# Kernel optimization log

Measured on AMD Instinct MI355X. Metric: run time of the kernel, lower is better.

Reference implementation:

```python
import jax, jax.numpy as jnp
import numpy as np

B, SST, SL = 16, 256, 48
VOCAB, D, CH = 16384, 64, 112
TPI = 0.0


def setup_inputs() -> dict:
    key = jax.random.key(0)
    ks = jax.random.split(key, 26)
    def n(k, shp, s=0.05):
        return jax.random.normal(k, shp, dtype=jnp.float32) * s
    return {
        "x": jax.random.randint(ks[0], (B, SST), 0, VOCAB),
        "ees": n(ks[1], (B, D, SL), 1.0),
        "emb": n(ks[2], (VOCAB, D)),
        "cl0_w": n(ks[3], (CH, D, 1)),  "cl0_b": n(ks[4], (CH,)),
        "cl1_w": n(ks[5], (CH, CH, 3)), "cl1_b": n(ks[6], (CH,)),
        "claa_w": n(ks[7], (CH, CH, 3)), "claa_b": n(ks[8], (CH,)),
        "clfa_w": n(ks[9], (CH, CH, 3)), "clfa_b": n(ks[10], (CH,)),
        "ccac_w": n(ks[11], (CH, CH, 3)), "ccac_b": n(ks[12], (CH,)),
        "cib_w": n(ks[13], (D, CH, 1)),  "cib_b": n(ks[14], (D,)),
        "cpr1_w": n(ks[15], (D, 2 * D, 1)), "cpr1_b": n(ks[16], (D,)),
        "cpr2_w": n(ks[17], (D, D, 1)),  "cpr2_b": n(ks[18], (D,)),
        "cma_w": n(ks[19], (CH, D, 1)),  "cma_b": n(ks[20], (CH,)),
        "ccf_w": n(ks[21], (D, CH, 1)),  "ccf_b": n(ks[22], (D,)),
        "fff_b": n(ks[23], (VOCAB,)),
    }


def _conv1x1(x, w, b):
    # x: [B,C,S], w: [O,C,1] -> [B,O,S]
    return jnp.einsum('oc,bcs->bos', w[:, :, 0], x) + b[None, :, None]


def _conv3(x, w, b):
    # valid 1D conv, channels-first. x: [B,C,S+2] -> [B,O,S]
    y = jax.lax.conv_general_dilated(x, w, (1,), 'VALID',
                                     dimension_numbers=('NCH', 'OIH', 'NCH'))
    return y + b[None, :, None]


def _forward(x, ees, emb, cl0_w, cl0_b, cl1_w, cl1_b, claa_w, claa_b,
             clfa_w, clfa_b, ccac_w, ccac_b, cib_w, cib_b,
             cpr1_w, cpr1_b, cpr2_w, cpr2_b, cma_w, cma_b,
             ccf_w, ccf_b, fff_b):
    b = x.shape[0]
    pre_d = jnp.transpose(emb[x], (0, 2, 1))            # [B,64,SST]
    t = _conv1x1(pre_d, cl0_w, cl0_b)                   # [B,112,SST]
    tp = jnp.full((b, CH, 2), TPI, dtype=t.dtype)       # tpi pad columns

    # split cpr layer1 weight into the t-half and ees-half (concat along ch)
    wt, we = cpr1_w[:, :D, 0], cpr1_w[:, D:, 0]

    def stage(t_in, conv_w, conv_b):
        tt = jnp.concatenate([tp, t_in], axis=2)        # [B,112,SST+2]
        xconv = jax.nn.relu(_conv3(tt, conv_w, conv_b))  # [B,112,SST]
        c = _conv1x1(xconv, cib_w, cib_b)               # [B,64,SST]
        # all-pairs broadcast (sl x sst) + 1x1-conv MLP, equivalent to
        # repeat/concat/cpr in the original, without duplicating data
        h = (jnp.einsum('oc,bcs->bos', wt, c)[:, :, None, :]
             + jnp.einsum('oc,bcl->bol', we, ees)[:, :, :, None]
             + cpr1_b[None, :, None, None])             # [B,64,SL,SST]
        h = jax.nn.relu(h)
        h = jax.nn.relu(jnp.einsum('oc,bcls->bols', cpr2_w[:, :, 0], h)
                        + cpr2_b[None, :, None, None])
        m = jnp.max(h, axis=2)                          # max over sl -> [B,64,SST]
        return _conv1x1(m, cma_w, cma_b) + xconv        # residual add

    t = stage(t, cl1_w, cl1_b)
    t = stage(t, claa_w, claa_b)
    t = stage(t, clfa_w, clfa_b)
    t = stage(t, ccac_w, ccac_b)

    ccf_out = _conv1x1(t, ccf_w, ccf_b)                 # [B,64,SST]
    # tied-weight output projection: [B,SST,64] @ emb.T -> [B,SST,VOCAB]
    output = jnp.einsum('bds,vd->bsv', ccf_out, emb) + fff_b
    return output, pre_d, ccf_out


def reference(x, ees, emb, cl0_w, cl0_b, cl1_w, cl1_b, claa_w, claa_b,
              clfa_w, clfa_b, ccac_w, ccac_b, cib_w, cib_b,
              cpr1_w, cpr1_b, cpr2_w, cpr2_b, cma_w, cma_b,
              ccf_w, ccf_b, fff_b):
    return _forward(x, ees, emb, cl0_w, cl0_b, cl1_w, cl1_b, claa_w, claa_b,
                    clfa_w, clfa_b, ccac_w, ccac_b, cib_w, cib_b,
                    cpr1_w, cpr1_b, cpr2_w, cpr2_b, cma_w, cma_b,
                    ccf_w, ccf_b, fff_b)
```

## Files before the change

### kernel.cpp

```cpp
#include <hip/hip_runtime.h>

#define B_ 16
#define SST 256
#define SL 48
#define VOCAB 16384
#define D_ 64
#define CH 112

#define OUT0_ELEMS ((size_t)B_*SST*VOCAB)
#define OUT1_ELEMS (B_*D_*SST)

typedef __attribute__((ext_vector_type(8))) short s8v;
typedef __attribute__((ext_vector_type(4))) float f32x4;

#define MFMA(a,b,c) __builtin_amdgcn_mfma_f32_16x16x32_bf16(a, b, c, 0, 0, 0)

__device__ __forceinline__ void split1(float f, unsigned short* h, unsigned short* l) {
    unsigned u = __float_as_uint(f);
    *h = (unsigned short)(u >> 16);
    float lo = f - __uint_as_float(u & 0xffff0000u);
    *l = (unsigned short)(__float_as_uint(lo) >> 16);
}
__device__ __forceinline__ uint2 split_pack2(float f0, float f1) {
    unsigned u0 = __float_as_uint(f0), u1 = __float_as_uint(f1);
    unsigned hp = (u0 >> 16) | (u1 & 0xffff0000u);
    float l0 = f0 - __uint_as_float(u0 & 0xffff0000u);
    float l1 = f1 - __uint_as_float(u1 & 0xffff0000u);
    unsigned lp = (__float_as_uint(l0) >> 16) | (__float_as_uint(l1) & 0xffff0000u);
    return make_uint2(hp, lp);
}

__global__ void e_kernel(const float* __restrict__ ees,
                         const float* __restrict__ cpr1_w,
                         const float* __restrict__ cpr1_b,
                         const float* __restrict__ cib_b,
                         float* __restrict__ Eb) {
    int bl = blockIdx.x;
    int b = bl / SL, l = bl % SL;
    int tid = threadIdx.x;
    __shared__ float ec[D_];
    ec[tid] = ees[(b*D_ + tid)*SL + l];
    __syncthreads();
    const float* wrow = cpr1_w + tid*(2*D_);
    float acc = cpr1_b[tid];
    #pragma unroll
    for (int k = 0; k < D_; ++k) acc += wrow[k]*cib_b[k];
    #pragma unroll
    for (int c = 0; c < D_; ++c) acc += wrow[D_ + c]*ec[c];
    Eb[(b*SL + l)*D_ + tid] = acc;
}

__global__ void emb2bf_kernel(const float* __restrict__ emb,
                              unsigned short* __restrict__ hi,
                              unsigned short* __restrict__ lo) {
    int i = blockIdx.x*256 + threadIdx.x;
    float4 v = reinterpret_cast<const float4*>(emb)[i];
    ushort4 h, l;
    split1(v.x, &h.x, &l.x);
    split1(v.y, &h.y, &l.y);
    split1(v.z, &h.z, &l.z);
    split1(v.w, &h.w, &l.w);
    reinterpret_cast<ushort4*>(hi)[i] = h;
    reinterpret_cast<ushort4*>(lo)[i] = l;
}

__global__ void conv_prep_kernel(const float* __restrict__ w0, const float* __restrict__ w1,
                                 const float* __restrict__ w2, const float* __restrict__ w3,
                                 unsigned short* __restrict__ Wch, unsigned short* __restrict__ Wcl) {
    int gid = blockIdx.x*256 + threadIdx.x;
    int c = gid & 127;
    int o = (gid >> 7) & 127;
    int kst = gid >> 14;
    int k = kst % 3, st = kst / 3;
    const float* w = (st == 0) ? w0 : (st == 1) ? w1 : (st == 2) ? w2 : w3;
    float v = (o < CH && c < CH) ? w[o*CH*3 + c*3 + k] : 0.f;
    unsigned short h, l; split1(v, &h, &l);
    Wch[gid] = h; Wcl[gid] = l;
}

__global__ void shared_prep_kernel(const float* __restrict__ cpr1_w,
                                   const float* __restrict__ cib_w,
                                   const float* __restrict__ cpr2_w,
                                   const float* __restrict__ cma_w,
                                   const float* __restrict__ ccf_w,
                                   const float* __restrict__ cl0_w,
                                   unsigned short* __restrict__ Wcomb_h, unsigned short* __restrict__ Wcomb_l,
                                   unsigned short* __restrict__ W2h, unsigned short* __restrict__ W2l,
                                   unsigned short* __restrict__ cmah, unsigned short* __restrict__ cmal,
                                   unsigned short* __restrict__ ccfh, unsigned short* __restrict__ ccfl,
                                   unsigned short* __restrict__ cl0h, unsigned short* __restrict__ cl0l) {
    int gid = blockIdx.x*256 + threadIdx.x;
    unsigned short h, l;
    if (gid < 8192) {
        int o = gid >> 7, c = gid & 127;
        float v = 0.f;
        if (c < CH) {
            const float* wrow = cpr1_w + o*(2*D_);
            #pragma unroll
            for (int k = 0; k < D_; ++k) v += wrow[k]*cib_w[k*CH + c];
        }
        split1(v, &h, &l); Wcomb_h[gid] = h; Wcomb_l[gid] = l;
    } else if (gid < 12288) {
        int idx = gid - 8192;
        split1(cpr2_w[idx], &h, &l); W2h[idx] = h; W2l[idx] = l;
    } else if (gid < 20480) {
        int idx = gid - 12288;
        int o = idx >> 6;
        float v = (o < CH) ? cma_w[idx] : 0.f;
        split1(v, &h, &l); cmah[idx] = h; cmal[idx] = l;
    } else if (gid < 28672) {
        int idx = gid - 20480;
        int d = idx >> 7, c = idx & 127;
        float v = (c < CH) ? ccf_w[d*CH + c] : 0.f;
        split1(v, &h, &l); ccfh[idx] = h; ccfl[idx] = l;
    } else {
        int idx = gid - 28672;
        int o = idx >> 6;
        float v = (o < CH) ? cl0_w[idx] : 0.f;
        split1(v, &h, &l); cl0h[idx] = h; cl0l[idx] = l;
    }
}

__device__ __forceinline__ void h2max_wave(
    const float* __restrict__ AcRow,
    const float* __restrict__ El,
    const unsigned short* __restrict__ W2h, const unsigned short* __restrict__ W2l,
    int n, int kg, int o_lane, float b2_lane,
    unsigned short* __restrict__ Mmh, unsigned short* __restrict__ Mml, int bs) {
    float4 a00 = *reinterpret_cast<const float4*>(AcRow + kg*8);
    float4 a01 = *reinterpret_cast<const float4*>(AcRow + kg*8 + 4);
    float4 a10 = *reinterpret_cast<const float4*>(AcRow + 32 + kg*8);
    float4 a11 = *reinterpret_cast<const float4*>(AcRow + 32 + kg*8 + 4);

    f32x4 acc[4][3];
    #pragma unroll
    for (int mt = 0; mt < 4; ++mt)
        #pragma unroll
        for (int lt = 0; lt < 3; ++lt)
            acc[mt][lt] = (f32x4){0.f, 0.f, 0.f, 0.f};

    #pragma unroll
    for (int kt = 0; kt < 2; ++kt) {
        int cc = kt*32 + kg*8;
        float4 aA = (kt == 0) ? a00 : a10;
        float4 aB = (kt == 0) ? a01 : a11;
        s8v a2h[4], a2l[4];
        #pragma unroll
        for (int mt = 0; mt < 4; ++mt) {
            a2h[mt] = *(const s8v*)&W2h[(mt*16 + n)*64 + cc];
            a2l[mt] = *(const s8v*)&W2l[(mt*16 + n)*64 + cc];
        }
        #pragma unroll
        for (int lt = 0; lt < 3; ++lt) {
            const float* ep = &El[(lt*16 + n)*68 + cc];
            float4 e0 = *reinterpret_cast<const float4*>(ep);
            float4 e1 = *reinterpret_cast<const float4*>(ep + 4);
            float h0 = fmaxf(aA.x + e0.x, 0.f);
            float h1 = fmaxf(aA.y + e0.y, 0.f);
            float h2 = fmaxf(aA.z + e0.z, 0.f);
            float h3 = fmaxf(aA.w + e0.w, 0.f);
            float h4 = fmaxf(aB.x + e1.x, 0.f);
            float h5 = fmaxf(aB.y + e1.y, 0.f);
            float h6 = fmaxf(aB.z + e1.z, 0.f);
            float h7 = fmaxf(aB.w + e1.w, 0.f);
            uint2 q0 = split_pack2(h0, h1);
            uint2 q1 = split_pack2(h2, h3);
            uint2 q2 = split_pack2(h4, h5);
            uint2 q3 = split_pack2(h6, h7);
            union { unsigned u[4]; s8v v; } Bh, Bl;
            Bh.u[0] = q0.x; Bh.u[1] = q1.x; Bh.u[2] = q2.x; Bh.u[3] = q3.x;
            Bl.u[0] = q0.y; Bl.u[1] = q1.y; Bl.u[2] = q2.y; Bl.u[3] = q3.y;
            #pragma unroll
            for (int mt = 0; mt < 4; ++mt) {
                acc[mt][lt] = MFMA(a2h[mt], Bh.v, acc[mt][lt]);
                acc[mt][lt] = MFMA(a2h[mt], Bl.v, acc[mt][lt]);
                acc[mt][lt] = MFMA(a2l[mt], Bh.v, acc[mt][lt]);
            }
        }
    }

    float mx[16];
    #pragma unroll
    for (int mt = 0; mt < 4; ++mt)
        #pragma unroll
        for (int r = 0; r < 4; ++r)
            mx[mt*4 + r] = fmaxf(fmaxf(acc[mt][0][r], acc[mt][1][r]), acc[mt][2][r]);
    #pragma unroll
    for (int step = 0; step < 4; ++step) {
        int msk = 1 << step;
        #pragma unroll
        for (int i = 0; i < 16; ++i)
            mx[i] = fmaxf(mx[i], __shfl_xor(mx[i], msk));
    }
    float sel = mx[0];
    #pragma unroll
    for (int i = 1; i < 16; ++i)
        sel = (n == i) ? mx[i] : sel;
    float mval = fmaxf(sel + b2_lane, 0.f);
    unsigned short mh, ml; split1(mval, &mh, &ml);
    Mmh[bs*64 + o_lane] = mh;
    Mml[bs*64 + o_lane] = ml;
}

__global__ __launch_bounds__(512) void stage1_kernel(
    const int* __restrict__ x, const float* __restrict__ emb,
    const unsigned short* __restrict__ cl0h, const unsigned short* __restrict__ cl0l,
    const float* __restrict__ cl0_b,
    const unsigned short* __restrict__ Wch, const unsigned short* __restrict__ Wcl,
    const float* __restrict__ conv_b,
    const unsigned short* __restrict__ Wcombh, const unsigned short* __restrict__ Wcombl,
    const float* __restrict__ Eb,
    const unsigned short* __restrict__ W2h, const unsigned short* __restrict__ W2l,
    const float* __restrict__ cpr2_b,
    float* __restrict__ pre_d, float* __restrict__ xc_g,
    unsigned short* __restrict__ Mmh, unsigned short* __restrict__ Mml) {
    int b = blockIdx.x >> 4, s0 = (blockIdx.x & 15) << 4;
    int tid = threadIdx.x, w = tid >> 6, lane = tid & 63, n = lane & 15, kg = lane >> 4;

    __shared__ unsigned short Eg_h[18*72], Eg_l[18*72];
    __shared__ unsigned short Tt_h[18*136], Tt_l[18*136];
    __shared__ unsigned short Xt_h[16*136], Xt_l[16*136];
    __shared__ float El[48*68];
    __shared__ float AcT[16*68];

    for (int idx = tid; idx < 288; idx += 512) {
        int si = idx >> 4, c4 = (idx & 15)*4;
        int s = s0 - 2 + si;
        float4 v = make_float4(0.f, 0.f, 0.f, 0.f);
        if (s >= 0) {
            int tok = x[b*SST + s];
            v = *reinterpret_cast<const float4*>(&emb[tok*D_ + c4]);
        }
        ushort4 h, l;
        split1(v.x, &h.x, &l.x); split1(v.y, &h.y, &l.y);
        split1(v.z, &h.z, &l.z); split1(v.w, &h.w, &l.w);
        *reinterpret_cast<ushort4*>(&Eg_h[si*72 + c4]) = h;
        *reinterpret_cast<ushort4*>(&Eg_l[si*72 + c4]) = l;
        if (si >= 2) {
            pre_d[(b*D_ + c4+0)*SST + s] = v.x;
            pre_d[(b*D_ + c4+1)*SST + s] = v.y;
            pre_d[(b*D_ + c4+2)*SST + s] = v.z;
            pre_d[(b*D_ + c4+3)*SST + s] = v.w;
        }
    }
    for (int idx = tid; idx < 768; idx += 512) {
        int l = idx >> 4, c4 = (idx & 15)*4;
        *reinterpret_cast<float4*>(&El[l*68 + c4]) =
            *reinterpret_cast<const float4*>(&Eb[(b*SL + l)*64 + c4]);
    }
    __syncthreads();

    int ob = w*16 + kg*4;
    #pragma unroll
    for (int ct = 0; ct < 2; ++ct) {
        int si = ct*2 + n;
        f32x4 tv = {0.f, 0.f, 0.f, 0.f};
        #pragma unroll
        for (int kt = 0; kt < 2; ++kt) {
            int cc = kt*32 + kg*8;
            s8v bh = *(const s8v*)&Eg_h[si*72 + cc];
            s8v bl = *(const s8v*)&Eg_l[si*72 + cc];
            int ai = (w*16 + n)*64 + cc;
            s8v ah = *(const s8v*)&cl0h[ai];
            s8v al = *(const s8v*)&cl0l[ai];
            tv = MFMA(ah, bh, tv); tv = MFMA(ah, bl, tv); tv = MFMA(al, bh, tv);
        }
        int s = s0 - 2 + si;
        float r0 = 0.f, r1 = 0.f, r2 = 0.f, r3 = 0.f;
        if (s >= 0) {
            r0 = tv[0] + ((ob+0 < CH) ? cl0_b[ob+0] : 0.f);
            r1 = tv[1] + ((ob+1 < CH) ? cl0_b[ob+1] : 0.f);
            r2 = tv[2] + ((ob+2 < CH) ? cl0_b[ob+2] : 0.f);
            r3 = tv[3] + ((ob+3 < CH) ? cl0_b[ob+3] : 0.f);
        }
        uint2 p01 = split_pack2(r0, r1), p23 = split_pack2(r2, r3);
        *reinterpret_cast<uint2*>(&Tt_h[si*136 + ob]) = make_uint2(p01.x, p23.x);
        *reinterpret_cast<uint2*>(&Tt_l[si*136 + ob]) = make_uint2(p01.y, p23.y);
    }
    __syncthreads();

    f32x4 xcv = {0.f, 0.f, 0.f, 0.f};
    #pragma unroll
    for (int k = 0; k < 3; ++k)
        #pragma unroll
        for (int kt = 0; kt < 4; ++kt) {
            int cc = kt*32 + kg*8;
            s8v bh = *(const s8v*)&Tt_h[(n + k)*136 + cc];
            s8v bl = *(const s8v*)&Tt_l[(n + k)*136 + cc];
            int ai = (k*128 + w*16 + n)*128 + cc;
            s8v ah = *(const s8v*)&Wch[ai];
            s8v al = *(const s8v*)&Wcl[ai];
            xcv = MFMA(ah, bh, xcv); xcv = MFMA(ah, bl, xcv); xcv = MFMA(al, bh, xcv);
        }
    #pragma unroll
    for (int r = 0; r < 4; ++r) {
        float cb = (ob + r < CH) ? conv_b[ob + r] : 0.f;
        xcv[r] = fmaxf(xcv[r] + cb, 0.f);
    }
    {
        uint2 p01 = split_pack2(xcv[0], xcv[1]), p23 = split_pack2(xcv[2], xcv[3]);
        *reinterpret_cast<uint2*>(&Xt_h[n*136 + ob]) = make_uint2(p01.x, p23.x);
        *reinterpret_cast<uint2*>(&Xt_l[n*136 + ob]) = make_uint2(p01.y, p23.y);
        *reinterpret_cast<float4*>(&xc_g[(b*SST + s0 + n)*128 + ob]) =
            make_float4(xcv[0], xcv[1], xcv[2], xcv[3]);
    }
    __syncthreads();

    if (w < 4) {
        f32x4 acc = {0.f, 0.f, 0.f, 0.f};
        #pragma unroll
        for (int kt = 0; kt < 4; ++kt) {
            int cc = kt*32 + kg*8;
            int ai = (w*16 + n)*128 + cc;
            s8v ah = *(const s8v*)&Wcombh[ai];
            s8v al = *(const s8v*)&Wcombl[ai];
            s8v bh = *(const s8v*)&Xt_h[n*136 + cc];
            s8v bl = *(const s8v*)&Xt_l[n*136 + cc];
            acc = MFMA(ah, bh, acc); acc = MFMA(ah, bl, acc); acc = MFMA(al, bh, acc);
        }
        *reinterpret_cast<float4*>(&AcT[n*68 + w*16 + kg*4]) =
            make_float4(acc[0], acc[1], acc[2], acc[3]);
    }
    __syncthreads();

    int o_lane = ((n >> 2) << 4) + (kg << 2) + (n & 3);
    float b2_lane = cpr2_b[o_lane];
    #pragma unroll
    for (int si = 0; si < 2; ++si) {
        int s = w*2 + si;
        h2max_wave(&AcT[s*68], El, W2h, W2l, n, kg, o_lane, b2_lane,
                   Mmh, Mml, b*SST + s0 + s);
    }
}

__global__ __launch_bounds__(512) void stagem_kernel(
    const unsigned short* __restrict__ Mmh_in, const unsigned short* __restrict__ Mml_in,
    const unsigned short* __restrict__ cmah, const unsigned short* __restrict__ cmal,
    const float* __restrict__ cma_b, const float* __restrict__ xc_prev,
    const unsigned short* __restrict__ Wch, const unsigned short* __restrict__ Wcl,
    const float* __restrict__ conv_b,
    const unsigned short* __restrict__ Wcombh, const unsigned short* __restrict__ Wcombl,
    const float* __restrict__ Eb,
    const unsigned short* __restrict__ W2h, const unsigned short* __restrict__ W2l,
    const float* __restrict__ cpr2_b,
    float* __restrict__ xc_g,
    unsigned short* __restrict__ Mmh_out, unsigned short* __restrict__ Mml_out) {
    int b = blockIdx.x >> 4, s0 = (blockIdx.x & 15) << 4;
    int tid = threadIdx.x, w = tid >> 6, lane = tid & 63, n = lane & 15, kg = lane >> 4;

    __shared__ unsigned short Eg_h[18*72], Eg_l[18*72];
    __shared__ unsigned short Tt_h[18*136], Tt_l[18*136];
    __shared__ unsigned short Xt_h[16*136], Xt_l[16*136];
    __shared__ float El[48*68];
    __shared__ float AcT[16*68];

    for (int idx = tid; idx < 288; idx += 512) {
        int si = idx >> 4, c4 = (idx & 15)*4;
        int s = s0 - 2 + si;
        uint2 h = make_uint2(0, 0), l = make_uint2(0, 0);
        if (s >= 0) {
            h = *reinterpret_cast<const uint2*>(&Mmh_in[(b*SST + s)*64 + c4]);
            l = *reinterpret_cast<const uint2*>(&Mml_in[(b*SST + s)*64 + c4]);
        }
        *reinterpret_cast<uint2*>(&Eg_h[si*72 + c4]) = h;
        *reinterpret_cast<uint2*>(&Eg_l[si*72 + c4]) = l;
    }
    for (int idx = tid; idx < 768; idx += 512) {
        int l = idx >> 4, c4 = (idx & 15)*4;
        *reinterpret_cast<float4*>(&El[l*68 + c4]) =
            *reinterpret_cast<const float4*>(&Eb[(b*SL + l)*64 + c4]);
    }
    __syncthreads();

    int ob = w*16 + kg*4;
    #pragma unroll
    for (int ct = 0; ct < 2; ++ct) {
        int si = ct*2 + n;
        f32x4 tv = {0.f, 0.f, 0.f, 0.f};
        #pragma unroll
        for (int kt = 0; kt < 2; ++kt) {
            int cc = kt*32 + kg*8;
            s8v bh = *(const s8v*)&Eg_h[si*72 + cc];
            s8v bl = *(const s8v*)&Eg_l[si*72 + cc];
            int ai = (w*16 + n)*64 + cc;
            s8v ah = *(const s8v*)&cmah[ai];
            s8v al = *(const s8v*)&cmal[ai];
            tv = MFMA(ah, bh, tv); tv = MFMA(ah, bl, tv); tv = MFMA(al, bh, tv);
        }
        int s = s0 - 2 + si;
        float r0 = 0.f, r1 = 0.f, r2 = 0.f, r3 = 0.f;
        if (s >= 0) {
            float4 xr = *reinterpret_cast<const float4*>(&xc_prev[(b*SST + s)*128 + ob]);
            r0 = tv[0] + ((ob+0 < CH) ? cma_b[ob+0] : 0.f) + xr.x;
            r1 = tv[1] + ((ob+1 < CH) ? cma_b[ob+1] : 0.f) + xr.y;
            r2 = tv[2] + ((ob+2 < CH) ? cma_b[ob+2] : 0.f) + xr.z;
            r3 = tv[3] + ((ob+3 < CH) ? cma_b[ob+3] : 0.f) + xr.w;
        }
        uint2 p01 = split_pack2(r0, r1), p23 = split_pack2(r2, r3);
        *reinterpret_cast<uint2*>(&Tt_h[si*136 + ob]) = make_uint2(p01.x, p23.x);
        *reinterpret_cast<uint2*>(&Tt_l[si*136 + ob]) = make_uint2(p01.y, p23.y);
    }
    __syncthreads();

    f32x4 xcv = {0.f, 0.f, 0.f, 0.f};
    #pragma unroll
    for (int k = 0; k < 3; ++k)
        #pragma unroll
        for (int kt = 0; kt < 4; ++kt) {
            int cc = kt*32 + kg*8;
            s8v bh = *(const s8v*)&Tt_h[(n + k)*136 + cc];
            s8v bl = *(const s8v*)&Tt_l[(n + k)*136 + cc];
            int ai = (k*128 + w*16 + n)*128 + cc;
            s8v ah = *(const s8v*)&Wch[ai];
            s8v al = *(const s8v*)&Wcl[ai];
            xcv = MFMA(ah, bh, xcv); xcv = MFMA(ah, bl, xcv); xcv = MFMA(al, bh, xcv);
        }
    #pragma unroll
    for (int r = 0; r < 4; ++r) {
        float cb = (ob + r < CH) ? conv_b[ob + r] : 0.f;
        xcv[r] = fmaxf(xcv[r] + cb, 0.f);
    }
    {
        uint2 p01 = split_pack2(xcv[0], xcv[1]), p23 = split_pack2(xcv[2], xcv[3]);
        *reinterpret_cast<uint2*>(&Xt_h[n*136 + ob]) = make_uint2(p01.x, p23.x);
        *reinterpret_cast<uint2*>(&Xt_l[n*136 + ob]) = make_uint2(p01.y, p23.y);
        *reinterpret_cast<float4*>(&xc_g[(b*SST + s0 + n)*128 + ob]) =
            make_float4(xcv[0], xcv[1], xcv[2], xcv[3]);
    }
    __syncthreads();

    if (w < 4) {
        f32x4 acc = {0.f, 0.f, 0.f, 0.f};
        #pragma unroll
        for (int kt = 0; kt < 4; ++kt) {
            int cc = kt*32 + kg*8;
            int ai = (w*16 + n)*128 + cc;
            s8v ah = *(const s8v*)&Wcombh[ai];
            s8v al = *(const s8v*)&Wcombl[ai];
            s8v bh = *(const s8v*)&Xt_h[n*136 + cc];
            s8v bl = *(const s8v*)&Xt_l[n*136 + cc];
            acc = MFMA(ah, bh, acc); acc = MFMA(ah, bl, acc); acc = MFMA(al, bh, acc);
        }
        *reinterpret_cast<float4*>(&AcT[n*68 + w*16 + kg*4]) =
            make_float4(acc[0], acc[1], acc[2], acc[3]);
    }
    __syncthreads();

    int o_lane = ((n >> 2) << 4) + (kg << 2) + (n & 3);
    float b2_lane = cpr2_b[o_lane];
    #pragma unroll
    for (int si = 0; si < 2; ++si) {
        int s = w*2 + si;
        h2max_wave(&AcT[s*68], El, W2h, W2l, n, kg, o_lane, b2_lane,
                   Mmh_out, Mml_out, b*SST + s0 + s);
    }
}

__global__ __launch_bounds__(256) void cmaccf_kernel(
    const unsigned short* __restrict__ Mmh, const unsigned short* __restrict__ Mml,
    const unsigned short* __restrict__ cmah, const unsigned short* __restrict__ cmal,
    const float* __restrict__ cma_b, const float* __restrict__ xc_prev,
    const unsigned short* __restrict__ ccfh, const unsigned short* __restrict__ ccfl,
    const float* __restrict__ ccf_b,
    float* __restrict__ ccf_out,
    unsigned short* __restrict__ Ahi, unsigned short* __restrict__ Alo) {
    int b = blockIdx.x >> 4, s0 = (blockIdx.x & 15) << 4;
    int tid = threadIdx.x, w = tid >> 6, lane = tid & 63, n = lane & 15, kg = lane >> 4;

    __shared__ unsigned short Mh[16*72], Ml[16*72];
    __shared__ unsigned short Th[16*136], Tl[16*136];

    for (int idx = tid; idx < 256; idx += 256) {
        int s = idx >> 4, c4 = (idx & 15)*4;
        *reinterpret_cast<uint2*>(&Mh[s*72 + c4]) =
            *reinterpret_cast<const uint2*>(&Mmh[(b*SST + s0 + s)*64 + c4]);
        *reinterpret_cast<uint2*>(&Ml[s*72 + c4]) =
            *reinterpret_cast<const uint2*>(&Mml[(b*SST + s0 + s)*64 + c4]);
    }
    __syncthreads();

    #pragma unroll
    for (int half = 0; half < 2; ++half) {
        int ob = (half*4 + w)*16 + kg*4;
        f32x4 tv = {0.f, 0.f, 0.f, 0.f};
        #pragma unroll
        for (int kt = 0; kt < 2; ++kt) {
            int cc = kt*32 + kg*8;
            s8v bh = *(const s8v*)&Mh[n*72 + cc];
            s8v bl = *(const s8v*)&Ml[n*72 + cc];
            int ai = ((half*4 + w)*16 + n)*64 + cc;
            s8v ah = *(const s8v*)&cmah[ai];
            s8v al = *(const s8v*)&cmal[ai];
            tv = MFMA(ah, bh, tv); tv = MFMA(ah, bl, tv); tv = MFMA(al, bh, tv);
        }
        int s = s0 + n;
        float4 xr = *reinterpret_cast<const float4*>(&xc_prev[(b*SST + s)*128 + ob]);
        float r0 = tv[0] + ((ob+0 < CH) ? cma_b[ob+0] : 0.f) + xr.x;
        float r1 = tv[1] + ((ob+1 < CH) ? cma_b[ob+1] : 0.f) + xr.y;
        float r2 = tv[2] + ((ob+2 < CH) ? cma_b[ob+2] : 0.f) + xr.z;
        float r3 = tv[3] + ((ob+3 < CH) ? cma_b[ob+3] : 0.f) + xr.w;
        uint2 p01 = split_pack2(r0, r1), p23 = split_pack2(r2, r3);
        *reinterpret_cast<uint2*>(&Th[n*136 + ob]) = make_uint2(p01.x, p23.x);
        *reinterpret_cast<uint2*>(&Tl[n*136 + ob]) = make_uint2(p01.y, p23.y);
    }
    __syncthreads();

    f32x4 acc = {0.f, 0.f, 0.f, 0.f};
    #pragma unroll
    for (int kt = 0; kt < 4; ++kt) {
        int cc = kt*32 + kg*8;
        int ai = (w*16 + n)*128 + cc;
        s8v ah = *(const s8v*)&ccfh[ai];
        s8v al = *(const s8v*)&ccfl[ai];
        s8v bh = *(const s8v*)&Th[n*136 + cc];
        s8v bl = *(const s8v*)&Tl[n*136 + cc];
        acc = MFMA(ah, bh, acc); acc = MFMA(ah, bl, acc); acc = MFMA(al, bh, acc);
    }
    int d0 = w*16 + kg*4, s = s0 + n;
    float v0 = acc[0] + ccf_b[d0+0];
    float v1 = acc[1] + ccf_b[d0+1];
    float v2 = acc[2] + ccf_b[d0+2];
    float v3 = acc[3] + ccf_b[d0+3];
    ccf_out[(b*D_ + d0+0)*SST + s] = v0;
    ccf_out[(b*D_ + d0+1)*SST + s] = v1;
    ccf_out[(b*D_ + d0+2)*SST + s] = v2;
    ccf_out[(b*D_ + d0+3)*SST + s] = v3;
    uint2 p01 = split_pack2(v0, v1), p23 = split_pack2(v2, v3);
    *reinterpret_cast<uint2*>(&Ahi[(b*SST + s)*64 + d0]) = make_uint2(p01.x, p23.x);
    *reinterpret_cast<uint2*>(&Alo[(b*SST + s)*64 + d0]) = make_uint2(p01.y, p23.y);
}

__global__ __launch_bounds__(256) void logits_mfma_kernel(
    const unsigned short* __restrict__ Ahi,
    const unsigned short* __restrict__ Alo,
    const unsigned short* __restrict__ Bhi,
    const unsigned short* __restrict__ Blo,
    const float* __restrict__ fffb,
    float* __restrict__ out) {
    int ntile = blockIdx.x & 127;
    int mtile = blockIdx.x >> 7;
    int wid = threadIdx.x >> 6;
    int lane = threadIdx.x & 63;
    int wm = wid >> 1, wn = wid & 1;
    int m0 = mtile*128 + wm*64;
    int v0 = ntile*128 + wn*64;
    int row16 = lane & 15, kg = lane >> 4;

    const short* Ah = (const short*)Ahi;
    const short* Al = (const short*)Alo;
    const short* Bh = (const short*)Bhi;
    const short* Bl = (const short*)Blo;

    f32x4 acc[4][4];
    #pragma unroll
    for (int mi = 0; mi < 4; ++mi)
        #pragma unroll
        for (int ni = 0; ni < 4; ++ni)
            acc[mi][ni] = (f32x4){0.f, 0.f, 0.f, 0.f};

    #pragma unroll
    for (int kk = 0; kk < 2; ++kk) {
        int koff = kk*32 + kg*8;
        s8v ah[4], al[4], bh[4], bl[4];
        #pragma unroll
        for (int mi = 0; mi < 4; ++mi) {
            int r = (m0 + mi*16 + row16)*D_ + koff;
            ah[mi] = *reinterpret_cast<const s8v*>(Ah + r);
            al[mi] = *reinterpret_cast<const s8v*>(Al + r);
        }
        #pragma unroll
        for (int ni = 0; ni < 4; ++ni) {
            int r = (v0 + ni*16 + row16)*D_ + koff;
            bh[ni] = *reinterpret_cast<const s8v*>(Bh + r);
            bl[ni] = *reinterpret_cast<const s8v*>(Bl + r);
        }
        #pragma unroll
        for (int mi = 0; mi < 4; ++mi)
            #pragma unroll
            for (int ni = 0; ni < 4; ++ni) {
                acc[mi][ni] = MFMA(ah[mi], bh[ni], acc[mi][ni]);
                acc[mi][ni] = MFMA(ah[mi], bl[ni], acc[mi][ni]);
                acc[mi][ni] = MFMA(al[mi], bh[ni], acc[mi][ni]);
            }
    }

    float fb[4];
    #pragma unroll
    for (int ni = 0; ni < 4; ++ni) fb[ni] = fffb[v0 + ni*16 + row16];

    #pragma unroll
    for (int mi = 0; mi < 4; ++mi) {
        #pragma unroll
        for (int r = 0; r < 4; ++r) {
            size_t rowbase = (size_t)(m0 + mi*16 + kg*4 + r)*VOCAB;
            #pragma unroll
            for (int ni = 0; ni < 4; ++ni) {
                out[rowbase + v0 + ni*16 + row16] = acc[mi][ni][r] + fb[ni];
            }
        }
    }
}

extern "C" void kernel_launch(void* const* d_in, const int* in_sizes, int n_in,
                              void* d_out, int out_size, void* d_ws, size_t ws_size,
                              hipStream_t stream) {
    const int*   x     = (const int*)d_in[0];
    const float* ees   = (const float*)d_in[1];
    const float* emb   = (const float*)d_in[2];
    const float* cl0_w = (const float*)d_in[3];
    const float* cl0_b = (const float*)d_in[4];
    const float* cl1_w = (const float*)d_in[5];
    const float* cl1_b = (const float*)d_in[6];
    const float* claa_w= (const float*)d_in[7];
    const float* claa_b= (const float*)d_in[8];
    const float* clfa_w= (const float*)d_in[9];
    const float* clfa_b= (const float*)d_in[10];
    const float* ccac_w= (const float*)d_in[11];
    const float* ccac_b= (const float*)d_in[12];
    const float* cib_w = (const float*)d_in[13];
    const float* cib_b = (const float*)d_in[14];
    const float* cpr1_w= (const float*)d_in[15];
    const float* cpr1_b= (const float*)d_in[16];
    const float* cpr2_w= (const float*)d_in[17];
    const float* cpr2_b= (const float*)d_in[18];
    const float* cma_w = (const float*)d_in[19];
    const float* cma_b = (const float*)d_in[20];
    const float* ccf_w = (const float*)d_in[21];
    const float* ccf_b = (const float*)d_in[22];
    const float* fff_b = (const float*)d_in[23];

    float* out = (float*)d_out;
    float* out_pre = out + OUT0_ELEMS;
    float* out_ccf = out_pre + OUT1_ELEMS;

    unsigned short* EmbHi = (unsigned short*)d_ws;
    unsigned short* EmbLo = EmbHi + VOCAB*D_;
    unsigned short* Ahi   = EmbLo + VOCAB*D_;
    unsigned short* Alo   = Ahi + B_*SST*D_;

    char* sc = (char*)d_out + (size_t)16*1024*1024;
    float*          Eb    = (float*)sc;            sc += B_*SL*D_*4;
    unsigned short* Wch   = (unsigned short*)sc;   sc += 4*3*128*128*2;
    unsigned short* Wcl   = (unsigned short*)sc;   sc += 4*3*128*128*2;
    unsigned short* Wcombh= (unsigned short*)sc;   sc += 64*128*2;
    unsigned short* Wcombl= (unsigned short*)sc;   sc += 64*128*2;
    unsigned short* W2h   = (unsigned short*)sc;   sc += 64*64*2;
    unsigned short* W2l   = (unsigned short*)sc;   sc += 64*64*2;
    unsigned short* cmah  = (unsigned short*)sc;   sc += 128*64*2;
    unsigned short* cmal  = (unsigned short*)sc;   sc += 128*64*2;
    unsigned short* ccfh  = (unsigned short*)sc;   sc += 64*128*2;
    unsigned short* ccfl  = (unsigned short*)sc;   sc += 64*128*2;
    unsigned short* cl0h  = (unsigned short*)sc;   sc += 128*64*2;
    unsigned short* cl0l  = (unsigned short*)sc;   sc += 128*64*2;
    float*          xc_a  = (float*)sc;            sc += (size_t)B_*SST*128*4;
    float*          xc_b  = (float*)sc;            sc += (size_t)B_*SST*128*4;
    unsigned short* Mmh   = (unsigned short*)sc;   sc += B_*SST*64*2;
    unsigned short* Mml   = (unsigned short*)sc;   sc += B_*SST*64*2;

    conv_prep_kernel<<<768, 256, 0, stream>>>(cl1_w, claa_w, clfa_w, ccac_w, Wch, Wcl);
    shared_prep_kernel<<<144, 256, 0, stream>>>(cpr1_w, cib_w, cpr2_w, cma_w, ccf_w, cl0_w,
        Wcombh, Wcombl, W2h, W2l, cmah, cmal, ccfh, ccfl, cl0h, cl0l);
    emb2bf_kernel<<<VOCAB*D_/4/256, 256, 0, stream>>>(emb, EmbHi, EmbLo);
    e_kernel<<<B_*SL, 64, 0, stream>>>(ees, cpr1_w, cpr1_b, cib_b, Eb);

    const int WCS = 3*128*128;
    stage1_kernel<<<256, 512, 0, stream>>>(x, emb, cl0h, cl0l, cl0_b,
        Wch + 0*WCS, Wcl + 0*WCS, cl1_b, Wcombh, Wcombl, Eb, W2h, W2l, cpr2_b,
        out_pre, xc_a, Mmh, Mml);
    stagem_kernel<<<256, 512, 0, stream>>>(Mmh, Mml, cmah, cmal, cma_b, xc_a,
        Wch + 1*WCS, Wcl + 1*WCS, claa_b, Wcombh, Wcombl, Eb, W2h, W2l, cpr2_b,
        xc_b, Mmh, Mml);
    stagem_kernel<<<256, 512, 0, stream>>>(Mmh, Mml, cmah, cmal, cma_b, xc_b,
        Wch + 2*WCS, Wcl + 2*WCS, clfa_b, Wcombh, Wcombl, Eb, W2h, W2l, cpr2_b,
        xc_a, Mmh, Mml);
    stagem_kernel<<<256, 512, 0, stream>>>(Mmh, Mml, cmah, cmal, cma_b, xc_a,
        Wch + 3*WCS, Wcl + 3*WCS, ccac_b, Wcombh, Wcombl, Eb, W2h, W2l, cpr2_b,
        xc_b, Mmh, Mml);

    cmaccf_kernel<<<256, 256, 0, stream>>>(Mmh, Mml, cmah, cmal, cma_b, xc_b,
        ccfh, ccfl, ccf_b, out_ccf, Ahi, Alo);
    logits_mfma_kernel<<<(B_*SST/128)*(VOCAB/128), 256, 0, stream>>>(
        Ahi, Alo, EmbHi, EmbLo, fff_b, out);
}
```

Measured before the change: 170.3 us.

## Merge prep kernels into one launch and fuse last stage with cma/ccf epilogue

Four weight/embedding preparation kernels are combined into a single launch that selects its work by block index. The last conv stage is fused with the cma residual and ccf projection into a new stage4 kernel. That kernel keeps the max-pooled features in shared memory and writes the logits operands directly, so the xc_b and Mm global round trip and two launches go away. The cost is a larger kernel with more shared memory and barriers, which could lower occupancy.

```diff
diff --git a/kernel.cpp b/kernel.cpp
--- a/kernel.cpp
+++ b/kernel.cpp
@@ -6,6 +6,7 @@
 #define VOCAB 16384
 #define D_ 64
 #define CH 112
+#define WCS (3*128*128)
 
 #define OUT0_ELEMS ((size_t)B_*SST*VOCAB)
 #define OUT1_ELEMS (B_*D_*SST)
@@ -30,94 +31,88 @@
     return make_uint2(hp, lp);
 }
 
-__global__ void e_kernel(const float* __restrict__ ees,
-                         const float* __restrict__ cpr1_w,
-                         const float* __restrict__ cpr1_b,
-                         const float* __restrict__ cib_b,
-                         float* __restrict__ Eb) {
-    int bl = blockIdx.x;
-    int b = bl / SL, l = bl % SL;
-    int tid = threadIdx.x;
-    __shared__ float ec[D_];
-    ec[tid] = ees[(b*D_ + tid)*SL + l];
-    __syncthreads();
-    const float* wrow = cpr1_w + tid*(2*D_);
-    float acc = cpr1_b[tid];
-    #pragma unroll
-    for (int k = 0; k < D_; ++k) acc += wrow[k]*cib_b[k];
-    #pragma unroll
-    for (int c = 0; c < D_; ++c) acc += wrow[D_ + c]*ec[c];
-    Eb[(b*SL + l)*D_ + tid] = acc;
-}
-
-__global__ void emb2bf_kernel(const float* __restrict__ emb,
-                              unsigned short* __restrict__ hi,
-                              unsigned short* __restrict__ lo) {
-    int i = blockIdx.x*256 + threadIdx.x;
-    float4 v = reinterpret_cast<const float4*>(emb)[i];
-    ushort4 h, l;
-    split1(v.x, &h.x, &l.x);
-    split1(v.y, &h.y, &l.y);
-    split1(v.z, &h.z, &l.z);
-    split1(v.w, &h.w, &l.w);
-    reinterpret_cast<ushort4*>(hi)[i] = h;
-    reinterpret_cast<ushort4*>(lo)[i] = l;
-}
-
-__global__ void conv_prep_kernel(const float* __restrict__ w0, const float* __restrict__ w1,
-                                 const float* __restrict__ w2, const float* __restrict__ w3,
-                                 unsigned short* __restrict__ Wch, unsigned short* __restrict__ Wcl) {
-    int gid = blockIdx.x*256 + threadIdx.x;
-    int c = gid & 127;
-    int o = (gid >> 7) & 127;
-    int kst = gid >> 14;
-    int k = kst % 3, st = kst / 3;
-    const float* w = (st == 0) ? w0 : (st == 1) ? w1 : (st == 2) ? w2 : w3;
-    float v = (o < CH && c < CH) ? w[o*CH*3 + c*3 + k] : 0.f;
-    unsigned short h, l; split1(v, &h, &l);
-    Wch[gid] = h; Wcl[gid] = l;
-}
-
-__global__ void shared_prep_kernel(const float* __restrict__ cpr1_w,
-                                   const float* __restrict__ cib_w,
-                                   const float* __restrict__ cpr2_w,
-                                   const float* __restrict__ cma_w,
-                                   const float* __restrict__ ccf_w,
-                                   const float* __restrict__ cl0_w,
-                                   unsigned short* __restrict__ Wcomb_h, unsigned short* __restrict__ Wcomb_l,
-                                   unsigned short* __restrict__ W2h, unsigned short* __restrict__ W2l,
-                                   unsigned short* __restrict__ cmah, unsigned short* __restrict__ cmal,
-                                   unsigned short* __restrict__ ccfh, unsigned short* __restrict__ ccfl,
-                                   unsigned short* __restrict__ cl0h, unsigned short* __restrict__ cl0l) {
-    int gid = blockIdx.x*256 + threadIdx.x;
+__global__ __launch_bounds__(256) void prep_kernel(
+    const float* __restrict__ w0, const float* __restrict__ w1,
+    const float* __restrict__ w2, const float* __restrict__ w3,
+    unsigned short* __restrict__ Wch, unsigned short* __restrict__ Wcl,
+    const float* __restrict__ cpr1_w, const float* __restrict__ cib_w,
+    const float* __restrict__ cpr2_w, const float* __restrict__ cma_w,
+    const float* __restrict__ ccf_w, const float* __restrict__ cl0_w,
+    unsigned short* __restrict__ Wcomb_h, unsigned short* __restrict__ Wcomb_l,
+    unsigned short* __restrict__ W2h, unsigned short* __restrict__ W2l,
+    unsigned short* __restrict__ cmah, unsigned short* __restrict__ cmal,
+    unsigned short* __restrict__ ccfh, unsigned short* __restrict__ ccfl,
+    unsigned short* __restrict__ cl0h, unsigned short* __restrict__ cl0l,
+    const float* __restrict__ emb,
+    unsigned short* __restrict__ EmbHi, unsigned short* __restrict__ EmbLo,
+    const float* __restrict__ ees, const float* __restrict__ cpr1_b,
+    const float* __restrict__ cib_b, float* __restrict__ Eb) {
+    int blk = blockIdx.x, tid = threadIdx.x;
     unsigned short h, l;
-    if (gid < 8192) {
-        int o = gid >> 7, c = gid & 127;
-        float v = 0.f;
-        if (c < CH) {
-            const float* wrow = cpr1_w + o*(2*D_);
-            #pragma unroll
-            for (int k = 0; k < D_; ++k) v += wrow[k]*cib_w[k*CH + c];
-        }
-        split1(v, &h, &l); Wcomb_h[gid] = h; Wcomb_l[gid] = l;
-    } else if (gid < 12288) {
-        int idx = gid - 8192;
-        split1(cpr2_w[idx], &h, &l); W2h[idx] = h; W2l[idx] = l;
-    } else if (gid < 20480) {
-        int idx = gid - 12288;
-        int o = idx >> 6;
-        float v = (o < CH) ? cma_w[idx] : 0.f;
-        split1(v, &h, &l); cmah[idx] = h; cmal[idx] = l;
-    } else if (gid < 28672) {
-        int idx = gid - 20480;
-        int d = idx >> 7, c = idx & 127;
-        float v = (c < CH) ? ccf_w[d*CH + c] : 0.f;
-        split1(v, &h, &l); ccfh[idx] = h; ccfl[idx] = l;
+    if (blk < 768) {
+        int gid = blk*256 + tid;
+        int c = gid & 127;
+        int o = (gid >> 7) & 127;
+        int kst = gid >> 14;
+        int k = kst % 3, st = kst / 3;
+        const float* w = (st == 0) ? w0 : (st == 1) ? w1 : (st == 2) ? w2 : w3;
+        float v = (o < CH && c < CH) ? w[o*CH*3 + c*3 + k] : 0.f;
+        split1(v, &h, &l);
+        Wch[gid] = h; Wcl[gid] = l;
+    } else if (blk < 912) {
+        int gid = (blk - 768)*256 + tid;
+        if (gid < 8192) {
+            int o = gid >> 7, c = gid & 127;
+            float v = 0.f;
+            if (c < CH) {
+                const float* wrow = cpr1_w + o*(2*D_);
+                #pragma unroll
+                for (int k = 0; k < D_; ++k) v += wrow[k]*cib_w[k*CH + c];
+            }
+            split1(v, &h, &l); Wcomb_h[gid] = h; Wcomb_l[gid] = l;
+        } else if (gid < 12288) {
+            int idx = gid - 8192;
+            split1(cpr2_w[idx], &h, &l); W2h[idx] = h; W2l[idx] = l;
+        } else if (gid < 20480) {
+            int idx = gid - 12288;
+            int o = idx >> 6;
+            float v = (o < CH) ? cma_w[idx] : 0.f;
+            split1(v, &h, &l); cmah[idx] = h; cmal[idx] = l;
+        } else if (gid < 28672) {
+            int idx = gid - 20480;
+            int d = idx >> 7, c = idx & 127;
+            float v = (c < CH) ? ccf_w[d*CH + c] : 0.f;
+            split1(v, &h, &l); ccfh[idx] = h; ccfl[idx] = l;
+        } else {
+            int idx = gid - 28672;
+            int o = idx >> 6;
+            float v = (o < CH) ? cl0_w[idx] : 0.f;
+            split1(v, &h, &l); cl0h[idx] = h; cl0l[idx] = l;
+        }
+    } else if (blk < 1936) {
+        int i = (blk - 912)*256 + tid;
+        float4 v = reinterpret_cast<const float4*>(emb)[i];
+        ushort4 hh, ll;
+        split1(v.x, &hh.x, &ll.x);
+        split1(v.y, &hh.y, &ll.y);
+        split1(v.z, &hh.z, &ll.z);
+        split1(v.w, &hh.w, &ll.w);
+        reinterpret_cast<ushort4*>(EmbHi)[i] = hh;
+        reinterpret_cast<ushort4*>(EmbLo)[i] = ll;
     } else {
-        int idx = gid - 28672;
-        int o = idx >> 6;
-        float v = (o < CH) ? cl0_w[idx] : 0.f;
-        split1(v, &h, &l); cl0h[idx] = h; cl0l[idx] = l;
+        __shared__ float ec[4][64];
+        int g = tid >> 6, c = tid & 63;
+        int bl = (blk - 1936)*4 + g;
+        int b = bl / SL, lq = bl % SL;
+        ec[g][c] = ees[(b*D_ + c)*SL + lq];
+        __syncthreads();
+        const float* wrow = cpr1_w + c*(2*D_);
+        float acc = cpr1_b[c];
+        #pragma unroll
+        for (int k = 0; k < D_; ++k) acc += wrow[k]*cib_b[k];
+        #pragma unroll
+        for (int cc = 0; cc < D_; ++cc) acc += wrow[D_ + cc]*ec[g][cc];
+        Eb[(b*SL + lq)*D_ + c] = acc;
     }
 }
 
@@ -126,7 +121,7 @@
     const float* __restrict__ El,
     const unsigned short* __restrict__ W2h, const unsigned short* __restrict__ W2l,
     int n, int kg, int o_lane, float b2_lane,
-    unsigned short* __restrict__ Mmh, unsigned short* __restrict__ Mml, int bs) {
+    unsigned short* Mmh, unsigned short* Mml, int bs, int stride) {
     float4 a00 = *reinterpret_cast<const float4*>(AcRow + kg*8);
     float4 a01 = *reinterpret_cast<const float4*>(AcRow + kg*8 + 4);
     float4 a10 = *reinterpret_cast<const float4*>(AcRow + 32 + kg*8);
@@ -198,8 +193,8 @@
         sel = (n == i) ? mx[i] : sel;
     float mval = fmaxf(sel + b2_lane, 0.f);
     unsigned short mh, ml; split1(mval, &mh, &ml);
-    Mmh[bs*64 + o_lane] = mh;
-    Mml[bs*64 + o_lane] = ml;
+    Mmh[bs*stride + o_lane] = mh;
+    Mml[bs*stride + o_lane] = ml;
 }
 
 __global__ __launch_bounds__(512) void stage1_kernel(
@@ -329,7 +324,7 @@
     for (int si = 0; si < 2; ++si) {
         int s = w*2 + si;
         h2max_wave(&AcT[s*68], El, W2h, W2l, n, kg, o_lane, b2_lane,
-                   Mmh, Mml, b*SST + s0 + s);
+                   Mmh, Mml, b*SST + s0 + s, 64);
     }
 }
 
@@ -452,14 +447,20 @@
     for (int si = 0; si < 2; ++si) {
         int s = w*2 + si;
         h2max_wave(&AcT[s*68], El, W2h, W2l, n, kg, o_lane, b2_lane,
-                   Mmh_out, Mml_out, b*SST + s0 + s);
-    }
-}
-
-__global__ __launch_bounds__(256) void cmaccf_kernel(
-    const unsigned short* __restrict__ Mmh, const unsigned short* __restrict__ Mml,
+                   Mmh_out, Mml_out, b*SST + s0 + s, 64);
+    }
+}
+
+__global__ __launch_bounds__(512) void stage4_kernel(
+    const unsigned short* __restrict__ Mmh_in, const unsigned short* __restrict__ Mml_in,
     const unsigned short* __restrict__ cmah, const unsigned short* __restrict__ cmal,
     const float* __restrict__ cma_b, const float* __restrict__ xc_prev,
+    const unsigned short* __restrict__ Wch, const unsigned short* __restrict__ Wcl,
+    const float* __restrict__ conv_b,
+    const unsigned short* __restrict__ Wcombh, const unsigned short* __restrict__ Wcombl,
+    const float* __restrict__ Eb,
+    const unsigned short* __restrict__ W2h, const unsigned short* __restrict__ W2l,
+    const float* __restrict__ cpr2_b,
     const unsigned short* __restrict__ ccfh, const unsigned short* __restrict__ ccfl,
     const float* __restrict__ ccf_b,
     float* __restrict__ ccf_out,
@@ -467,67 +468,159 @@
     int b = blockIdx.x >> 4, s0 = (blockIdx.x & 15) << 4;
     int tid = threadIdx.x, w = tid >> 6, lane = tid & 63, n = lane & 15, kg = lane >> 4;
 
-    __shared__ unsigned short Mh[16*72], Ml[16*72];
-    __shared__ unsigned short Th[16*136], Tl[16*136];
-
-    for (int idx = tid; idx < 256; idx += 256) {
-        int s = idx >> 4, c4 = (idx & 15)*4;
-        *reinterpret_cast<uint2*>(&Mh[s*72 + c4]) =
-            *reinterpret_cast<const uint2*>(&Mmh[(b*SST + s0 + s)*64 + c4]);
-        *reinterpret_cast<uint2*>(&Ml[s*72 + c4]) =
-            *reinterpret_cast<const uint2*>(&Mml[(b*SST + s0 + s)*64 + c4]);
-    }
-    __syncthreads();
-
-    #pragma unroll
-    for (int half = 0; half < 2; ++half) {
-        int ob = (half*4 + w)*16 + kg*4;
+    __shared__ unsigned short Eg_h[18*72], Eg_l[18*72];
+    __shared__ unsigned short Tt_h[18*136], Tt_l[18*136];
+    __shared__ unsigned short Xt_h[16*136], Xt_l[16*136];
+    __shared__ float El[48*68];
+    __shared__ float AcT[16*68];
+
+    for (int idx = tid; idx < 288; idx += 512) {
+        int si = idx >> 4, c4 = (idx & 15)*4;
+        int s = s0 - 2 + si;
+        uint2 h = make_uint2(0, 0), l = make_uint2(0, 0);
+        if (s >= 0) {
+            h = *reinterpret_cast<const uint2*>(&Mmh_in[(b*SST + s)*64 + c4]);
+            l = *reinterpret_cast<const uint2*>(&Mml_in[(b*SST + s)*64 + c4]);
+        }
+        *reinterpret_cast<uint2*>(&Eg_h[si*72 + c4]) = h;
+        *reinterpret_cast<uint2*>(&Eg_l[si*72 + c4]) = l;
+    }
+    for (int idx = tid; idx < 768; idx += 512) {
+        int l = idx >> 4, c4 = (idx & 15)*4;
+        *reinterpret_cast<float4*>(&El[l*68 + c4]) =
+            *reinterpret_cast<const float4*>(&Eb[(b*SL + l)*64 + c4]);
+    }
+    __syncthreads();
+
+    int ob = w*16 + kg*4;
+    #pragma unroll
+    for (int ct = 0; ct < 2; ++ct) {
+        int si = ct*2 + n;
         f32x4 tv = {0.f, 0.f, 0.f, 0.f};
         #pragma unroll
         for (int kt = 0; kt < 2; ++kt) {
             int cc = kt*32 + kg*8;
-            s8v bh = *(const s8v*)&Mh[n*72 + cc];
-            s8v bl = *(const s8v*)&Ml[n*72 + cc];
-            int ai = ((half*4 + w)*16 + n)*64 + cc;
+            s8v bh = *(const s8v*)&Eg_h[si*72 + cc];
+            s8v bl = *(const s8v*)&Eg_l[si*72 + cc];
+            int ai = (w*16 + n)*64 + cc;
             s8v ah = *(const s8v*)&cmah[ai];
             s8v al = *(const s8v*)&cmal[ai];
             tv = MFMA(ah, bh, tv); tv = MFMA(ah, bl, tv); tv = MFMA(al, bh, tv);
         }
-        int s = s0 + n;
-        float4 xr = *reinterpret_cast<const float4*>(&xc_prev[(b*SST + s)*128 + ob]);
-        float r0 = tv[0] + ((ob+0 < CH) ? cma_b[ob+0] : 0.f) + xr.x;
-        float r1 = tv[1] + ((ob+1 < CH) ? cma_b[ob+1] : 0.f) + xr.y;
-        float r2 = tv[2] + ((ob+2 < CH) ? cma_b[ob+2] : 0.f) + xr.z;
-        float r3 = tv[3] + ((ob+3 < CH) ? cma_b[ob+3] : 0.f) + xr.w;
+        int s = s0 - 2 + si;
+        float r0 = 0.f, r1 = 0.f, r2 = 0.f, r3 = 0.f;
+        if (s >= 0) {
+            float4 xr = *reinterpret_cast<const float4*>(&xc_prev[(b*SST + s)*128 + ob]);
+            r0 = tv[0] + ((ob+0 < CH) ? cma_b[ob+0] : 0.f) + xr.x;
+            r1 = tv[1] + ((ob+1 < CH) ? cma_b[ob+1] : 0.f) + xr.y;
+            r2 = tv[2] + ((ob+2 < CH) ? cma_b[ob+2] : 0.f) + xr.z;
+            r3 = tv[3] + ((ob+3 < CH) ? cma_b[ob+3] : 0.f) + xr.w;
+        }
         uint2 p01 = split_pack2(r0, r1), p23 = split_pack2(r2, r3);
-        *reinterpret_cast<uint2*>(&Th[n*136 + ob]) = make_uint2(p01.x, p23.x);
-        *reinterpret_cast<uint2*>(&Tl[n*136 + ob]) = make_uint2(p01.y, p23.y);
-    }
-    __syncthreads();
-
-    f32x4 acc = {0.f, 0.f, 0.f, 0.f};
-    #pragma unroll
-    for (int kt = 0; kt < 4; ++kt) {
-        int cc = kt*32 + kg*8;
-        int ai = (w*16 + n)*128 + cc;
-        s8v ah = *(const s8v*)&ccfh[ai];
-        s8v al = *(const s8v*)&ccfl[ai];
-        s8v bh = *(const s8v*)&Th[n*136 + cc];
-        s8v bl = *(const s8v*)&Tl[n*136 + cc];
-        acc = MFMA(ah, bh, acc); acc = MFMA(ah, bl, acc); acc = MFMA(al, bh, acc);
-    }
-    int d0 = w*16 + kg*4, s = s0 + n;
-    float v0 = acc[0] + ccf_b[d0+0];
-    float v1 = acc[1] + ccf_b[d0+1];
-    float v2 = acc[2] + ccf_b[d0+2];
-    float v3 = acc[3] + ccf_b[d0+3];
-    ccf_out[(b*D_ + d0+0)*SST + s] = v0;
-    ccf_out[(b*D_ + d0+1)*SST + s] = v1;
-    ccf_out[(b*D_ + d0+2)*SST + s] = v2;
-    ccf_out[(b*D_ + d0+3)*SST + s] = v3;
-    uint2 p01 = split_pack2(v0, v1), p23 = split_pack2(v2, v3);
-    *reinterpret_cast<uint2*>(&Ahi[(b*SST + s)*64 + d0]) = make_uint2(p01.x, p23.x);
-    *reinterpret_cast<uint2*>(&Alo[(b*SST + s)*64 + d0]) = make_uint2(p01.y, p23.y);
+        *reinterpret_cast<uint2*>(&Tt_h[si*136 + ob]) = make_uint2(p01.x, p23.x);
+        *reinterpret_cast<uint2*>(&Tt_l[si*136 + ob]) = make_uint2(p01.y, p23.y);
+    }
+    __syncthreads();
+
+    f32x4 xcv = {0.f, 0.f, 0.f, 0.f};
+    #pragma unroll
+    for (int k = 0; k < 3; ++k)
+        #pragma unroll
+        for (int kt = 0; kt < 4; ++kt) {
+            int cc = kt*32 + kg*8;
+            s8v bh = *(const s8v*)&Tt_h[(n + k)*136 + cc];
+            s8v bl = *(const s8v*)&Tt_l[(n + k)*136 + cc];
+            int ai = (k*128 + w*16 + n)*128 + cc;
+            s8v ah = *(const s8v*)&Wch[ai];
+            s8v al = *(const s8v*)&Wcl[ai];
+            xcv = MFMA(ah, bh, xcv); xcv = MFMA(ah, bl, xcv); xcv = MFMA(al, bh, xcv);
+        }
+    #pragma unroll
+    for (int r = 0; r < 4; ++r) {
+        float cb = (ob + r < CH) ? conv_b[ob + r] : 0.f;
+        xcv[r] = fmaxf(xcv[r] + cb, 0.f);
+    }
+    {
+        uint2 p01 = split_pack2(xcv[0], xcv[1]), p23 = split_pack2(xcv[2], xcv[3]);
+        *reinterpret_cast<uint2*>(&Xt_h[n*136 + ob]) = make_uint2(p01.x, p23.x);
+        *reinterpret_cast<uint2*>(&Xt_l[n*136 + ob]) = make_uint2(p01.y, p23.y);
+    }
+    __syncthreads();
+
+    if (w < 4) {
+        f32x4 acc = {0.f, 0.f, 0.f, 0.f};
+        #pragma unroll
+        for (int kt = 0; kt < 4; ++kt) {
+            int cc = kt*32 + kg*8;
+            int ai = (w*16 + n)*128 + cc;
+            s8v ah = *(const s8v*)&Wcombh[ai];
+            s8v al = *(const s8v*)&Wcombl[ai];
+            s8v bh = *(const s8v*)&Xt_h[n*136 + cc];
+            s8v bl = *(const s8v*)&Xt_l[n*136 + cc];
+            acc = MFMA(ah, bh, acc); acc = MFMA(ah, bl, acc); acc = MFMA(al, bh, acc);
+        }
+        *reinterpret_cast<float4*>(&AcT[n*68 + w*16 + kg*4]) =
+            make_float4(acc[0], acc[1], acc[2], acc[3]);
+    }
+    __syncthreads();
+
+    int o_lane = ((n >> 2) << 4) + (kg << 2) + (n & 3);
+    float b2_lane = cpr2_b[o_lane];
+    #pragma unroll
+    for (int si = 0; si < 2; ++si) {
+        int s = w*2 + si;
+        h2max_wave(&AcT[s*68], El, W2h, W2l, n, kg, o_lane, b2_lane,
+                   Eg_h, Eg_l, s, 72);
+    }
+    __syncthreads();
+
+    {
+        f32x4 tv = {0.f, 0.f, 0.f, 0.f};
+        #pragma unroll
+        for (int kt = 0; kt < 2; ++kt) {
+            int cc = kt*32 + kg*8;
+            s8v bh = *(const s8v*)&Eg_h[n*72 + cc];
+            s8v bl = *(const s8v*)&Eg_l[n*72 + cc];
+            int ai = (w*16 + n)*64 + cc;
+            s8v ah = *(const s8v*)&cmah[ai];
+            s8v al = *(const s8v*)&cmal[ai];
+            tv = MFMA(ah, bh, tv); tv = MFMA(ah, bl, tv); tv = MFMA(al, bh, tv);
+        }
+        float r0 = tv[0] + ((ob+0 < CH) ? cma_b[ob+0] : 0.f) + xcv[0];
+        float r1 = tv[1] + ((ob+1 < CH) ? cma_b[ob+1] : 0.f) + xcv[1];
+        float r2 = tv[2] + ((ob+2 < CH) ? cma_b[ob+2] : 0.f) + xcv[2];
+        float r3 = tv[3] + ((ob+3 < CH) ? cma_b[ob+3] : 0.f) + xcv[3];
+        uint2 p01 = split_pack2(r0, r1), p23 = split_pack2(r2, r3);
+        *reinterpret_cast<uint2*>(&Tt_h[n*136 + ob]) = make_uint2(p01.x, p23.x);
+        *reinterpret_cast<uint2*>(&Tt_l[n*136 + ob]) = make_uint2(p01.y, p23.y);
+    }
+    __syncthreads();
+
+    if (w < 4) {
+        f32x4 acc = {0.f, 0.f, 0.f, 0.f};
+        #pragma unroll
+        for (int kt = 0; kt < 4; ++kt) {
+            int cc = kt*32 + kg*8;
+            int ai = (w*16 + n)*128 + cc;
+            s8v ah = *(const s8v*)&ccfh[ai];
+            s8v al = *(const s8v*)&ccfl[ai];
+            s8v bh = *(const s8v*)&Tt_h[n*136 + cc];
+            s8v bl = *(const s8v*)&Tt_l[n*136 + cc];
+            acc = MFMA(ah, bh, acc); acc = MFMA(ah, bl, acc); acc = MFMA(al, bh, acc);
+        }
+        int d0 = w*16 + kg*4, s = s0 + n;
+        float v0 = acc[0] + ccf_b[d0+0];
+        float v1 = acc[1] + ccf_b[d0+1];
+        float v2 = acc[2] + ccf_b[d0+2];
+        float v3 = acc[3] + ccf_b[d0+3];
+        ccf_out[(b*D_ + d0+0)*SST + s] = v0;
+        ccf_out[(b*D_ + d0+1)*SST + s] = v1;
+        ccf_out[(b*D_ + d0+2)*SST + s] = v2;
+        ccf_out[(b*D_ + d0+3)*SST + s] = v3;
+        uint2 p01 = split_pack2(v0, v1), p23 = split_pack2(v2, v3);
+        *reinterpret_cast<uint2*>(&Ahi[(b*SST + s)*64 + d0]) = make_uint2(p01.x, p23.x);
+        *reinterpret_cast<uint2*>(&Alo[(b*SST + s)*64 + d0]) = make_uint2(p01.y, p23.y);
+    }
 }
 
 __global__ __launch_bounds__(256) void logits_mfma_kernel(
@@ -657,13 +750,13 @@
     unsigned short* Mmh   = (unsigned short*)sc;   sc += B_*SST*64*2;
     unsigned short* Mml   = (unsigned short*)sc;   sc += B_*SST*64*2;
 
-    conv_prep_kernel<<<768, 256, 0, stream>>>(cl1_w, claa_w, clfa_w, ccac_w, Wch, Wcl);
-    shared_prep_kernel<<<144, 256, 0, stream>>>(cpr1_w, cib_w, cpr2_w, cma_w, ccf_w, cl0_w,
-        Wcombh, Wcombl, W2h, W2l, cmah, cmal, ccfh, ccfl, cl0h, cl0l);
-    emb2bf_kernel<<<VOCAB*D_/4/256, 256, 0, stream>>>(emb, EmbHi, EmbLo);
-    e_kernel<<<B_*SL, 64, 0, stream>>>(ees, cpr1_w, cpr1_b, cib_b, Eb);
-
-    const int WCS = 3*128*128;
+    prep_kernel<<<2128, 256, 0, stream>>>(
+        cl1_w, claa_w, clfa_w, ccac_w, Wch, Wcl,
+        cpr1_w, cib_w, cpr2_w, cma_w, ccf_w, cl0_w,
+        Wcombh, Wcombl, W2h, W2l, cmah, cmal, ccfh, ccfl, cl0h, cl0l,
+        emb, EmbHi, EmbLo,
+        ees, cpr1_b, cib_b, Eb);
+
     stage1_kernel<<<256, 512, 0, stream>>>(x, emb, cl0h, cl0l, cl0_b,
         Wch + 0*WCS, Wcl + 0*WCS, cl1_b, Wcombh, Wcombl, Eb, W2h, W2l, cpr2_b,
         out_pre, xc_a, Mmh, Mml);
@@ -673,12 +766,10 @@
     stagem_kernel<<<256, 512, 0, stream>>>(Mmh, Mml, cmah, cmal, cma_b, xc_b,
         Wch + 2*WCS, Wcl + 2*WCS, clfa_b, Wcombh, Wcombl, Eb, W2h, W2l, cpr2_b,
         xc_a, Mmh, Mml);
-    stagem_kernel<<<256, 512, 0, stream>>>(Mmh, Mml, cmah, cmal, cma_b, xc_a,
+    stage4_kernel<<<256, 512, 0, stream>>>(Mmh, Mml, cmah, cmal, cma_b, xc_a,
         Wch + 3*WCS, Wcl + 3*WCS, ccac_b, Wcombh, Wcombl, Eb, W2h, W2l, cpr2_b,
-        xc_b, Mmh, Mml);
-
-    cmaccf_kernel<<<256, 256, 0, stream>>>(Mmh, Mml, cmah, cmal, cma_b, xc_b,
         ccfh, ccfl, ccf_b, out_ccf, Ahi, Alo);
+
     logits_mfma_kernel<<<(B_*SST/128)*(VOCAB/128), 256, 0, stream>>>(
         Ahi, Alo, EmbHi, EmbLo, fff_b, out);
 }
```

Measured after the change: 167.8 us (median of 2 runs). About the same (-1.5%).
